# Performance work log

Measured on AMD Instinct MI355X. Metric: run time of the kernel, lower is better.

Reference implementation:

```python
import jax, jax.numpy as jnp
import numpy as np

BATCH, SEQ, HID = 2, 384, 128
TABLE = 2 * SEQ + 1  # indices are diff + SEQ, diff in [-(SEQ-1), SEQ-1]


def setup_inputs() -> dict:
    key = jax.random.key(0)
    ks = jax.random.split(key, 8)
    pos_s = jax.random.randint(ks[0], (BATCH, SEQ), 0, SEQ, dtype=jnp.int64 if jax.config.jax_enable_x64 else jnp.int32)
    # span end >= span start, clipped to valid range
    span = jax.random.randint(ks[1], (BATCH, SEQ), 0, 8, dtype=pos_s.dtype)
    pos_e = jnp.minimum(pos_s + span, SEQ - 1)
    return {
        "pos_s": pos_s,
        "pos_e": pos_e,
        "pe_ss": jax.random.normal(ks[2], (TABLE, HID), dtype=jnp.float32),
        "pe_se": jax.random.normal(ks[3], (TABLE, HID), dtype=jnp.float32),
        "pe_es": jax.random.normal(ks[4], (TABLE, HID), dtype=jnp.float32),
        "pe_ee": jax.random.normal(ks[5], (TABLE, HID), dtype=jnp.float32),
        "W": jax.random.normal(ks[6], (HID, 4 * HID), dtype=jnp.float32) * (1.0 / np.sqrt(4 * HID)),
        "b": jnp.zeros((HID,), dtype=jnp.float32),
    }


def reference(pos_s, pos_e, pe_ss, pe_se, pe_es, pe_ee, W, b):
    S = pos_s.shape[1]
    # pairwise relative positions, shifted into table index range: [B, S, S]
    i_ss = pos_s[:, :, None] - pos_s[:, None, :] + S
    i_se = pos_s[:, :, None] - pos_e[:, None, :] + S
    i_es = pos_e[:, :, None] - pos_s[:, None, :] + S
    i_ee = pos_e[:, :, None] - pos_e[:, None, :] + S
    # gather 4 tables -> [B, S, S, H] each, concat -> [B, S, S, 4H]
    pe_4 = jnp.concatenate([pe_ss[i_ss], pe_se[i_se], pe_es[i_es], pe_ee[i_ee]], axis=-1)
    # Linear(4H -> H) + ReLU  (torch Linear: x @ W.T + b)
    rel = jnp.einsum('bqkf,hf->bqkh', pe_4, W) + b
    return jax.nn.relu(rel)
```

## Files before the change

kernel.cpp:

```cpp
#include <hip/hip_runtime.h>

#define BATCH 2
#define SEQ   384
#define HID   128
#define TABLE (2 * SEQ + 1)
#define KPB   8

__global__ void precompute_tables(const float* __restrict__ pe_ss,
                                  const float* __restrict__ pe_se,
                                  const float* __restrict__ pe_es,
                                  const float* __restrict__ pe_ee,
                                  const float* __restrict__ W,
                                  const float* __restrict__ b,
                                  float* __restrict__ T) {
    const int t   = blockIdx.x;
    const int tab = blockIdx.y;
    const int h   = threadIdx.x;

    const float* pe = (tab == 0) ? pe_ss : (tab == 1) ? pe_se
                    : (tab == 2) ? pe_es : pe_ee;

    __shared__ float s_pe[HID];
    s_pe[h] = pe[(size_t)t * HID + h];
    __syncthreads();

    const float4* w4 = (const float4*)(W + (size_t)h * (4 * HID) + tab * HID);
    const float4* p4 = (const float4*)s_pe;

    float acc = (tab == 0) ? b[h] : 0.0f;
#pragma unroll
    for (int f = 0; f < HID / 4; ++f) {
        float4 w = w4[f];
        float4 p = p4[f];
        acc += w.x * p.x + w.y * p.y + w.z * p.z + w.w * p.w;
    }
    T[((size_t)tab * TABLE + t) * HID + h] = acc;
}

__global__ void gather_fuse(const int* __restrict__ pos_s,
                            const int* __restrict__ pos_e,
                            const float* __restrict__ T,
                            float* __restrict__ out) {
    const int kk = threadIdx.x >> 5;
    const int h4 = threadIdx.x & 31;
    const int k  = blockIdx.x * KPB + kk;
    const int q  = blockIdx.y;
    const int bb = blockIdx.z;

    const int ps_q = pos_s[bb * SEQ + q];
    const int pe_q = pos_e[bb * SEQ + q];
    const int ps_k = pos_s[bb * SEQ + k];
    const int pe_k = pos_e[bb * SEQ + k];

    const int R = HID / 4;
    const float4* T4 = (const float4*)T;
    const size_t TR = (size_t)TABLE * R;

    float4 a = T4[         (size_t)(ps_q - ps_k + SEQ) * R + h4];
    float4 c = T4[    TR + (size_t)(ps_q - pe_k + SEQ) * R + h4];
    float4 d = T4[2 * TR + (size_t)(pe_q - ps_k + SEQ) * R + h4];
    float4 e = T4[3 * TR + (size_t)(pe_q - pe_k + SEQ) * R + h4];

    float4 r;
    r.x = fmaxf(a.x + c.x + d.x + e.x, 0.0f);
    r.y = fmaxf(a.y + c.y + d.y + e.y, 0.0f);
    r.z = fmaxf(a.z + c.z + d.z + e.z, 0.0f);
    r.w = fmaxf(a.w + c.w + d.w + e.w, 0.0f);

    ((float4*)out)[(((size_t)bb * SEQ + q) * SEQ + k) * R + h4] = r;
}

extern "C" void kernel_launch(void* const* d_in, const int* in_sizes, int n_in,
                              void* d_out, int out_size, void* d_ws, size_t ws_size,
                              hipStream_t stream) {
    const int*   pos_s = (const int*)d_in[0];
    const int*   pos_e = (const int*)d_in[1];
    const float* pe_ss = (const float*)d_in[2];
    const float* pe_se = (const float*)d_in[3];
    const float* pe_es = (const float*)d_in[4];
    const float* pe_ee = (const float*)d_in[5];
    const float* W     = (const float*)d_in[6];
    const float* b     = (const float*)d_in[7];
    float*       out   = (float*)d_out;
    float*       T     = (float*)d_ws;

    precompute_tables<<<dim3(TABLE, 4), HID, 0, stream>>>(
        pe_ss, pe_se, pe_es, pe_ee, W, b, T);

    gather_fuse<<<dim3(SEQ / KPB, SEQ, BATCH), 256, 0, stream>>>(
        pos_s, pos_e, T, out);
}
```

Measured before the change: 196.2 us.

## Transpose W, block table precompute over rows, use nontemporal output stores

Adds a kernel that transposes W so each thread reads coalesced weight columns. The table precompute now handles 8 table rows per block, reusing each weight load across those rows instead of issuing one block per row. The gather kernel writes its output with nontemporal stores so the large output stream bypasses cache retention. The change adds one extra kernel launch and a workspace region for the transposed weights.

```diff
diff --git a/kernel.cpp b/kernel.cpp
--- a/kernel.cpp
+++ b/kernel.cpp
@@ -5,36 +5,58 @@
 #define HID   128
 #define TABLE (2 * SEQ + 1)
 #define KPB   8
+#define TPB   8
+
+typedef float vfloat4 __attribute__((ext_vector_type(4)));
+
+
+__global__ void transpose_w(const float* __restrict__ W, float* __restrict__ Wt) {
+    const int idx = blockIdx.x * 256 + threadIdx.x;
+    const int h   = idx & (HID - 1);
+    const int f   = (idx >> 7) & (HID - 1);
+    const int tab = idx >> 14;
+    Wt[idx] = W[h * (4 * HID) + tab * HID + f];
+}
 
 __global__ void precompute_tables(const float* __restrict__ pe_ss,
                                   const float* __restrict__ pe_se,
                                   const float* __restrict__ pe_es,
                                   const float* __restrict__ pe_ee,
-                                  const float* __restrict__ W,
+                                  const float* __restrict__ Wt,
                                   const float* __restrict__ b,
                                   float* __restrict__ T) {
-    const int t   = blockIdx.x;
+    const int t0  = blockIdx.x * TPB;
     const int tab = blockIdx.y;
     const int h   = threadIdx.x;
 
     const float* pe = (tab == 0) ? pe_ss : (tab == 1) ? pe_se
                     : (tab == 2) ? pe_es : pe_ee;
 
-    __shared__ float s_pe[HID];
-    s_pe[h] = pe[(size_t)t * HID + h];
-    __syncthreads();
+    const float* pr[TPB];
+#pragma unroll
+    for (int r = 0; r < TPB; ++r) {
+        int tr = t0 + r; if (tr > TABLE - 1) tr = TABLE - 1;
+        pr[r] = pe + (size_t)tr * HID;
+    }
 
-    const float4* w4 = (const float4*)(W + (size_t)h * (4 * HID) + tab * HID);
-    const float4* p4 = (const float4*)s_pe;
+    float acc[TPB];
+    const float binit = (tab == 0) ? b[h] : 0.0f;
+#pragma unroll
+    for (int r = 0; r < TPB; ++r) acc[r] = binit;
 
-    float acc = (tab == 0) ? b[h] : 0.0f;
+    const float* wcol = Wt + ((size_t)tab * HID) * HID + h;
+#pragma unroll 4
+    for (int f = 0; f < HID; ++f) {
+        const float wf = wcol[(size_t)f * HID];
 #pragma unroll
-    for (int f = 0; f < HID / 4; ++f) {
-        float4 w = w4[f];
-        float4 p = p4[f];
-        acc += w.x * p.x + w.y * p.y + w.z * p.z + w.w * p.w;
+        for (int r = 0; r < TPB; ++r) acc[r] += pr[r][f] * wf;
     }
-    T[((size_t)tab * TABLE + t) * HID + h] = acc;
+
+#pragma unroll
+    for (int r = 0; r < TPB; ++r) {
+        const int t = t0 + r;
+        if (t < TABLE) T[((size_t)tab * TABLE + t) * HID + h] = acc[r];
+    }
 }
 
 __global__ void gather_fuse(const int* __restrict__ pos_s,
@@ -53,21 +75,23 @@
     const int pe_k = pos_e[bb * SEQ + k];
 
     const int R = HID / 4;
-    const float4* T4 = (const float4*)T;
+    const vfloat4* T4 = (const vfloat4*)T;
     const size_t TR = (size_t)TABLE * R;
 
-    float4 a = T4[         (size_t)(ps_q - ps_k + SEQ) * R + h4];
-    float4 c = T4[    TR + (size_t)(ps_q - pe_k + SEQ) * R + h4];
-    float4 d = T4[2 * TR + (size_t)(pe_q - ps_k + SEQ) * R + h4];
-    float4 e = T4[3 * TR + (size_t)(pe_q - pe_k + SEQ) * R + h4];
+    vfloat4 a = T4[         (size_t)(ps_q - ps_k + SEQ) * R + h4];
+    vfloat4 c = T4[    TR + (size_t)(ps_q - pe_k + SEQ) * R + h4];
+    vfloat4 d = T4[2 * TR + (size_t)(pe_q - ps_k + SEQ) * R + h4];
+    vfloat4 e = T4[3 * TR + (size_t)(pe_q - pe_k + SEQ) * R + h4];
 
-    float4 r;
-    r.x = fmaxf(a.x + c.x + d.x + e.x, 0.0f);
-    r.y = fmaxf(a.y + c.y + d.y + e.y, 0.0f);
-    r.z = fmaxf(a.z + c.z + d.z + e.z, 0.0f);
-    r.w = fmaxf(a.w + c.w + d.w + e.w, 0.0f);
+    vfloat4 s = a + c + d + e;
+    vfloat4 r;
+    r.x = fmaxf(s.x, 0.0f);
+    r.y = fmaxf(s.y, 0.0f);
+    r.z = fmaxf(s.z, 0.0f);
+    r.w = fmaxf(s.w, 0.0f);
 
-    ((float4*)out)[(((size_t)bb * SEQ + q) * SEQ + k) * R + h4] = r;
+    vfloat4* op = (vfloat4*)out + (((size_t)bb * SEQ + q) * SEQ + k) * R + h4;
+    __builtin_nontemporal_store(r, op);
 }
 
 extern "C" void kernel_launch(void* const* d_in, const int* in_sizes, int n_in,
@@ -82,10 +106,14 @@
     const float* W     = (const float*)d_in[6];
     const float* b     = (const float*)d_in[7];
     float*       out   = (float*)d_out;
-    float*       T     = (float*)d_ws;
 
-    precompute_tables<<<dim3(TABLE, 4), HID, 0, stream>>>(
-        pe_ss, pe_se, pe_es, pe_ee, W, b, T);
+    float* T  = (float*)d_ws;
+    float* Wt = T + (size_t)4 * TABLE * HID;
+
+    transpose_w<<<dim3((4 * HID * HID) / 256), 256, 0, stream>>>(W, Wt);
+
+    precompute_tables<<<dim3((TABLE + TPB - 1) / TPB, 4), HID, 0, stream>>>(
+        pe_ss, pe_se, pe_es, pe_ee, Wt, b, T);
 
     gather_fuse<<<dim3(SEQ / KPB, SEQ, BATCH), 256, 0, stream>>>(
         pos_s, pos_e, T, out);
```

New measurement: 196.1 us. Within noise of the previous version (-0.1%).
